# Kernel tuning notes

Measured on AMD Instinct MI355X. Metric: run time of the kernel, lower is better.

## Reference

```python
import jax, jax.numpy as jnp
import numpy as np
from jax import lax

BATCH, SEQ, D_FSQ = 8, 4096, 4
D_MODEL, D_STATE, D_CONV, L, OUT = 256, 16, 4, 2, 2
D_INNER = 2 * D_MODEL  # expand=2
EPS = 1e-5


def setup_inputs() -> dict:
    key = jax.random.key(0)
    ks = jax.random.split(key, 10)
    s = 0.02
    return {
        "z_seq": jax.random.normal(ks[0], (BATCH, SEQ, D_FSQ), jnp.float32),
        "ip_w": jax.random.normal(ks[1], (D_MODEL, D_FSQ), jnp.float32) * s,
        "ip_b": jnp.zeros((D_MODEL,), jnp.float32),
        "norm_g": jnp.ones((L, D_MODEL), jnp.float32),
        "norm_b": jnp.zeros((L, D_MODEL), jnp.float32),
        "inproj_w": jax.random.normal(ks[2], (L, 2 * D_INNER, D_MODEL), jnp.float32) * s,
        "conv_w": jax.random.normal(ks[3], (L, D_INNER, D_CONV), jnp.float32) * s,
        "conv_b": jnp.zeros((L, D_INNER), jnp.float32),
        "xproj_w": jax.random.normal(ks[4], (L, 2 * D_STATE + 1, D_INNER), jnp.float32) * s,
        "dt_w": jax.random.normal(ks[5], (L, D_INNER), jnp.float32) * s,
        "dt_b": jnp.zeros((L, D_INNER), jnp.float32),
        "outproj_w": jax.random.normal(ks[6], (L, D_MODEL, D_INNER), jnp.float32) * s,
        "onorm_g": jnp.ones((D_MODEL,), jnp.float32),
        "onorm_b": jnp.zeros((D_MODEL,), jnp.float32),
        "op_w": jax.random.normal(ks[7], (OUT, D_MODEL), jnp.float32) * s,
        "op_b": jnp.zeros((OUT,), jnp.float32),
    }


def _layernorm(x, g, b):
    mu = jnp.mean(x, axis=-1, keepdims=True)
    var = jnp.mean(jnp.square(x - mu), axis=-1, keepdims=True)
    return (x - mu) * lax.rsqrt(var + EPS) * g + b


def _selective_scan(x, dt, Bm, Cm):
    # x, dt: [B,T,d_inner]; Bm, Cm: [B,T,d_state]
    A = -jnp.arange(1, D_STATE + 1, dtype=x.dtype)  # [d_state]

    def step(h, inp):
        x_t, dt_t, B_t, C_t = inp  # [B,di],[B,di],[B,ds],[B,ds]
        A_bar = jnp.exp(dt_t[:, :, None] * A)            # [B,di,ds]
        h = A_bar * h + (dt_t * x_t)[:, :, None] * B_t[:, None, :]
        y_t = jnp.einsum("bds,bs->bd", h, C_t)
        return h, y_t

    xs = (jnp.swapaxes(x, 0, 1), jnp.swapaxes(dt, 0, 1),
          jnp.swapaxes(Bm, 0, 1), jnp.swapaxes(Cm, 0, 1))
    h0 = jnp.zeros((x.shape[0], D_INNER, D_STATE), x.dtype)
    _, ys = lax.scan(step, h0, xs)
    return jnp.swapaxes(ys, 0, 1)  # [B,T,d_inner]


def _block(x, g, b, Wi, cw, cb, Wx, dw, db, Wo):
    res = x
    x = _layernorm(x, g, b)
    xz = x @ Wi.T                               # [B,T,2*d_inner]
    xp, z = xz[..., :D_INNER], xz[..., D_INNER:]
    # causal depthwise conv1d (padding=d_conv-1 then truncate == left pad)
    xc = lax.conv_general_dilated(
        jnp.swapaxes(xp, 1, 2), cw[:, None, :], window_strides=(1,),
        padding=[(D_CONV - 1, 0)], dimension_numbers=("NCH", "OIH", "NCH"),
        feature_group_count=D_INNER) + cb[None, :, None]
    xc = jax.nn.silu(jnp.swapaxes(xc, 1, 2))    # [B,T,d_inner]
    ssm = xc @ Wx.T                             # [B,T,2*ds+1]
    Bm = ssm[..., :D_STATE]
    Cm = ssm[..., D_STATE:2 * D_STATE]
    dt_raw = ssm[..., 2 * D_STATE:]             # [B,T,1]
    dt = jax.nn.softplus(dt_raw * dw + db)      # Linear(1, d_inner)
    y = _selective_scan(xc, dt, Bm, Cm)
    y = y * jax.nn.silu(z)
    y = y @ Wo.T
    return y + res


def reference(z_seq, ip_w, ip_b, norm_g, norm_b, inproj_w, conv_w, conv_b,
              xproj_w, dt_w, dt_b, outproj_w, onorm_g, onorm_b, op_w, op_b):
    x = z_seq @ ip_w.T + ip_b
    for l in range(L):
        x = _block(x, norm_g[l], norm_b[l], inproj_w[l], conv_w[l], conv_b[l],
                   xproj_w[l], dt_w[l], dt_b[l], outproj_w[l])
    x = _layernorm(x, onorm_g, onorm_b)
    return x @ op_w.T + op_b
```

## Files before the change

### kernel.cpp

```cpp
#include <hip/hip_runtime.h>
#include <cstddef>
#include <cstdint>

#define DEV __device__ __forceinline__

namespace {
constexpr int BATCH = 8;
constexpr int SEQL  = 4096;
constexpr int DM    = 256;
constexpr int DS    = 16;
constexpr int DI    = 512;
constexpr int NTOK  = BATCH * SEQL;
constexpr int TC    = 64;
constexpr int NCH   = SEQL / TC;
constexpr float EPSF = 1e-5f;

constexpr size_t OFF_X   = 0;
constexpr size_t OFF_XPB = OFF_X   + (size_t)NTOK * DM * 4;
constexpr size_t OFF_ZBB = OFF_XPB + (size_t)NTOK * DI * 2;
constexpr size_t OFF_XCB = OFF_ZBB + (size_t)NTOK * DI * 2;
constexpr size_t OFF_XLN = OFF_XCB + (size_t)NTOK * DI * 2;
constexpr size_t OFF_B   = OFF_XLN + (size_t)NTOK * DM * 2;
constexpr size_t OFF_C   = OFF_B   + (size_t)NTOK * DS * 4;
constexpr size_t OFF_DTR = OFF_C   + (size_t)NTOK * DS * 4;
constexpr size_t OFF_HE  = OFF_DTR + (size_t)NTOK * 4;
constexpr size_t OFF_DTC = OFF_HE  + (size_t)BATCH * DI * NCH * DS * 4;
constexpr size_t OFF_WBI = OFF_DTC + (size_t)BATCH * DI * NCH * 4;
constexpr size_t OFF_WBO = OFF_WBI + (size_t)2 * 2 * DI * DM * 2;
constexpr size_t OFF_WBX = OFF_WBO + (size_t)2 * DM * DI * 2;
constexpr size_t OFF_CWT = OFF_WBX + (size_t)2 * 48 * DI * 2;
constexpr size_t WBI_EL  = 2 * 2 * DI * DM;
constexpr size_t WBO_EL  = 2 * DM * DI;
}

typedef __attribute__((ext_vector_type(8))) short short8;
typedef __attribute__((ext_vector_type(4))) float f32x4;

DEV float sigmoidf_(float v) { return 1.0f / (1.0f + __expf(-v)); }
DEV float siluf_(float v)    { return v * sigmoidf_(v); }
DEV float softplusf_(float v) {
    return fmaxf(v, 0.0f) + __logf(1.0f + __expf(-fabsf(v)));
}
DEV float b2f(unsigned short u) {
    union { unsigned int i; float f; } c; c.i = ((unsigned int)u) << 16; return c.f;
}
DEV float4 b4f(ushort4 u) {
    return make_float4(b2f(u.x), b2f(u.y), b2f(u.z), b2f(u.w));
}
DEV unsigned short f2b(float f) {
    union { float f; unsigned int i; } c; c.f = f;
    unsigned int lsb = (c.i >> 16) & 1u;
    c.i += 0x7fffu + lsb;
    return (unsigned short)(c.i >> 16);
}
DEV void pows16(float p, float* pb) {
    float p2 = p * p, p4 = p2 * p2, p8 = p4 * p4;
    pb[0] = p;        pb[1] = p2;       pb[2] = p2 * p;      pb[3] = p4;
    pb[4] = p4 * p;   pb[5] = p4 * p2;  pb[6] = p4 * p2 * p; pb[7] = p8;
    pb[8] = p8 * p;   pb[9] = p8 * p2;  pb[10] = p8 * p2 * p; pb[11] = p8 * p4;
    pb[12] = p8 * p4 * p; pb[13] = p8 * p4 * p2; pb[14] = p8 * p4 * p2 * p; pb[15] = p8 * p8;
}
DEV void gload_lds16(const unsigned short* g, unsigned short* l) {
    __builtin_amdgcn_global_load_lds(
        (__attribute__((address_space(1))) void*)(g),
        (__attribute__((address_space(3))) void*)(l), 16, 0, 0);
}

__global__ void k_cvt(const float* __restrict__ src, unsigned short* __restrict__ dst, int n) {
    int g = (blockIdx.x * 256 + threadIdx.x) * 4;
    if (g >= n) return;
    float4 v = *(const float4*)(src + g);
    ushort4 o;
    o.x = f2b(v.x); o.y = f2b(v.y); o.z = f2b(v.z); o.w = f2b(v.w);
    *(ushort4*)(dst + g) = o;
}

__global__ void k_cvtx(const float* __restrict__ src, unsigned short* __restrict__ dst) {
    int idx = blockIdx.x * 256 + threadIdx.x;
    int l = idx / (48 * 512), r = (idx >> 9) % 48, cc = idx & 511;
    dst[idx] = (r < 33) ? f2b(src[(size_t)(l * 33 + r) * 512 + cc]) : (unsigned short)0;
}

__global__ void k_cvtc(const float* __restrict__ src, float* __restrict__ dst) {
    int idx = blockIdx.x * 256 + threadIdx.x;
    int l = idx >> 11, k = (idx >> 9) & 3, d = idx & 511;
    dst[idx] = src[(size_t)(l * DI + d) * 4 + k];
}

__global__ void k_inproj(const float* __restrict__ z, const float* __restrict__ w,
                         const float* __restrict__ bias, float* __restrict__ x) {
    int g = blockIdx.x * 256 + threadIdx.x;
    int i = g >> 8, m = g & 255;
    float4 zv = *(const float4*)(z + (size_t)i * 4);
    float4 wv = *(const float4*)(w + (size_t)m * 4);
    float r = bias[m];
    r = fmaf(zv.x, wv.x, r);
    r = fmaf(zv.y, wv.y, r);
    r = fmaf(zv.z, wv.z, r);
    r = fmaf(zv.w, wv.w, r);
    x[g] = r;
}

__global__ void k_lnrow(const float* __restrict__ x, const float* __restrict__ gam,
                        const float* __restrict__ bet, unsigned short* __restrict__ xln) {
    int lane = threadIdx.x & 63, wid = threadIdx.x >> 6;
    int i = blockIdx.x * 4 + wid;
    float4 v = *(const float4*)(x + (size_t)i * DM + lane * 4);
    float s = v.x + v.y + v.z + v.w;
    float q = v.x * v.x + v.y * v.y + v.z * v.z + v.w * v.w;
    #pragma unroll
    for (int m = 32; m; m >>= 1) { s += __shfl_xor(s, m, 64); q += __shfl_xor(q, m, 64); }
    float mu = s * (1.0f / DM);
    float rs = rsqrtf(q * (1.0f / DM) - mu * mu + EPSF);
    float4 g4 = *(const float4*)(gam + lane * 4);
    float4 b4 = *(const float4*)(bet + lane * 4);
    ushort4 o;
    o.x = f2b((v.x - mu) * rs * g4.x + b4.x);
    o.y = f2b((v.y - mu) * rs * g4.y + b4.y);
    o.z = f2b((v.z - mu) * rs * g4.z + b4.z);
    o.w = f2b((v.w - mu) * rs * g4.w + b4.w);
    *(ushort4*)(xln + (size_t)i * DM + lane * 4) = o;
}

__global__ __launch_bounds__(256) void k_gemm1(
    const unsigned short* __restrict__ A, const unsigned short* __restrict__ W,
    unsigned short* __restrict__ xpb, unsigned short* __restrict__ zbb) {
    __shared__ unsigned short As[128 * 32];
    __shared__ unsigned short Bs[128 * 32];
    int tid = threadIdx.x, lane = tid & 63, wid = tid >> 6;
    int tileN = blockIdx.x & 7, tileM = blockIdx.x >> 3;
    int i0 = tileM * 128, n0 = tileN * 128;
    f32x4 acc[4][4];
    #pragma unroll
    for (int mi = 0; mi < 4; mi++)
        #pragma unroll
        for (int ni = 0; ni < 4; ni++) acc[mi][ni] = (f32x4){0.f, 0.f, 0.f, 0.f};

    int srow = (wid << 5) + (lane >> 2);
    int sblk = lane & 3;
    const unsigned short* ga = A + (size_t)(i0 + srow) * 256 + sblk * 8;
    const unsigned short* gb = W + (size_t)(n0 + srow) * 256 + sblk * 8;
    unsigned short* la = As + (wid << 5) * 32;
    unsigned short* lb = Bs + (wid << 5) * 32;
    int ar = lane & 15, ab = lane >> 4;
    const short8* pa = (const short8*)(As + ((wid >> 1) * 64 + ar) * 32 + ab * 8);
    const short8* pb = (const short8*)(Bs + ((wid & 1) * 64 + ar) * 32 + ab * 8);

    for (int k0 = 0; k0 < 256; k0 += 32) {
        gload_lds16(ga + k0,            la);
        gload_lds16(ga + k0 + 16 * 256, la + 16 * 32);
        gload_lds16(gb + k0,            lb);
        gload_lds16(gb + k0 + 16 * 256, lb + 16 * 32);
        __syncthreads();
        short8 a[4], b[4];
        #pragma unroll
        for (int mi = 0; mi < 4; mi++) a[mi] = pa[mi * 64];
        #pragma unroll
        for (int ni = 0; ni < 4; ni++) b[ni] = pb[ni * 64];
        #pragma unroll
        for (int mi = 0; mi < 4; mi++)
            #pragma unroll
            for (int ni = 0; ni < 4; ni++)
                acc[mi][ni] = __builtin_amdgcn_mfma_f32_16x16x32_bf16(a[mi], b[ni], acc[mi][ni], 0, 0, 0);
        __syncthreads();
    }
    int wr = wid >> 1, wc = wid & 1;
    int rbase = i0 + wr * 64 + (lane >> 4) * 4;
    int cbase = n0 + wc * 64 + (lane & 15);
    unsigned short* dst = (n0 < 512) ? xpb : zbb;
    int coff = (n0 < 512) ? cbase : cbase - 512;
    #pragma unroll
    for (int mi = 0; mi < 4; mi++)
        #pragma unroll
        for (int ni = 0; ni < 4; ni++)
            #pragma unroll
            for (int j = 0; j < 4; j++)
                dst[(size_t)(rbase + mi * 16 + j) * 512 + coff + ni * 16] = f2b(acc[mi][ni][j]);
}

__global__ void k_conv(const unsigned short* __restrict__ xpb, const float* __restrict__ cwT,
                       const float* __restrict__ cb, unsigned short* __restrict__ xcb) {
    int g = blockIdx.x * 256 + threadIdx.x;
    int tg = g >> 7, dq = g & 127;
    int d = dq * 4;
    int i0 = tg * 8;
    float4 w0 = *(const float4*)(cwT + 0 * DI + d);
    float4 w1 = *(const float4*)(cwT + 1 * DI + d);
    float4 w2 = *(const float4*)(cwT + 2 * DI + d);
    float4 w3 = *(const float4*)(cwT + 3 * DI + d);
    float4 bi = *(const float4*)(cb + d);
    float4 x0, x1, x2;
    if ((i0 & (SEQL - 1)) != 0) {
        x0 = b4f(*(const ushort4*)(xpb + (size_t)(i0 - 3) * DI + d));
        x1 = b4f(*(const ushort4*)(xpb + (size_t)(i0 - 2) * DI + d));
        x2 = b4f(*(const ushort4*)(xpb + (size_t)(i0 - 1) * DI + d));
    } else {
        x0 = x1 = x2 = make_float4(0.f, 0.f, 0.f, 0.f);
    }
    #pragma unroll
    for (int tt = 0; tt < 8; tt++) {
        float4 xc = b4f(*(const ushort4*)(xpb + (size_t)(i0 + tt) * DI + d));
        float4 a = bi;
        a.x = fmaf(w0.x, x0.x, a.x); a.y = fmaf(w0.y, x0.y, a.y);
        a.z = fmaf(w0.z, x0.z, a.z); a.w = fmaf(w0.w, x0.w, a.w);
        a.x = fmaf(w1.x, x1.x, a.x); a.y = fmaf(w1.y, x1.y, a.y);
        a.z = fmaf(w1.z, x1.z, a.z); a.w = fmaf(w1.w, x1.w, a.w);
        a.x = fmaf(w2.x, x2.x, a.x); a.y = fmaf(w2.y, x2.y, a.y);
        a.z = fmaf(w2.z, x2.z, a.z); a.w = fmaf(w2.w, x2.w, a.w);
        a.x = fmaf(w3.x, xc.x, a.x); a.y = fmaf(w3.y, xc.y, a.y);
        a.z = fmaf(w3.z, xc.z, a.z); a.w = fmaf(w3.w, xc.w, a.w);
        ushort4 o;
        o.x = f2b(siluf_(a.x)); o.y = f2b(siluf_(a.y));
        o.z = f2b(siluf_(a.z)); o.w = f2b(siluf_(a.w));
        *(ushort4*)(xcb + (size_t)(i0 + tt) * DI + d) = o;
        x0 = x1; x1 = x2; x2 = xc;
    }
}

__global__ __launch_bounds__(256) void k_xprojm(
    const unsigned short* __restrict__ A, const unsigned short* __restrict__ W,
    float* __restrict__ Bm, float* __restrict__ Cm, float* __restrict__ dtr) {
    __shared__ unsigned short As[128 * 32];
    __shared__ unsigned short Bs[48 * 32];
    int tid = threadIdx.x, lane = tid & 63, wid = tid >> 6;
    int i0 = blockIdx.x * 128;
    f32x4 acc[2][3];
    #pragma unroll
    for (int mi = 0; mi < 2; mi++)
        #pragma unroll
        for (int ni = 0; ni < 3; ni++) acc[mi][ni] = (f32x4){0.f, 0.f, 0.f, 0.f};

    int srow = lane >> 2, sblk = lane & 3;
    const unsigned short* ga = A + (size_t)(i0 + (wid << 5) + srow) * 512 + sblk * 8;
    unsigned short* la = As + (wid << 5) * 32;
    const unsigned short* gb = W + (size_t)((wid << 4) + srow) * 512 + sblk * 8;
    unsigned short* lb = Bs + (wid << 4) * 32;
    int ar = lane & 15, ab = lane >> 4;

    for (int k0 = 0; k0 < 512; k0 += 32) {
        gload_lds16(ga + k0,            la);
        gload_lds16(ga + k0 + 16 * 512, la + 16 * 32);
        if (wid < 3) gload_lds16(gb + k0, lb);
        __syncthreads();
        short8 a[2], b[3];
        #pragma unroll
        for (int mi = 0; mi < 2; mi++)
            a[mi] = *(const short8*)(As + ((wid << 5) + mi * 16 + ar) * 32 + ab * 8);
        #pragma unroll
        for (int ni = 0; ni < 3; ni++)
            b[ni] = *(const short8*)(Bs + (ni * 16 + ar) * 32 + ab * 8);
        #pragma unroll
        for (int mi = 0; mi < 2; mi++)
            #pragma unroll
            for (int ni = 0; ni < 3; ni++)
                acc[mi][ni] = __builtin_amdgcn_mfma_f32_16x16x32_bf16(a[mi], b[ni], acc[mi][ni], 0, 0, 0);
        __syncthreads();
    }
    #pragma unroll
    for (int mi = 0; mi < 2; mi++)
        #pragma unroll
        for (int ni = 0; ni < 3; ni++)
            #pragma unroll
            for (int j = 0; j < 4; j++) {
                int row = i0 + (wid << 5) + mi * 16 + (lane >> 4) * 4 + j;
                int ng = ni * 16 + (lane & 15);
                float v = acc[mi][ni][j];
                if (ng < 16)       Bm[(size_t)row * DS + ng] = v;
                else if (ng < 32)  Cm[(size_t)row * DS + ng - 16] = v;
                else if (ng == 32) dtr[row] = v;
            }
}

__global__ __launch_bounds__(256) void k_scan1(
    const unsigned short* __restrict__ xcb, const float* __restrict__ Bm,
    const float* __restrict__ dtr, const float* __restrict__ dw,
    const float* __restrict__ db, float* __restrict__ hend, float* __restrict__ dtc) {
    __shared__ float Bsh[64][16];
    __shared__ float dtl[64];
    int tid = threadIdx.x;
    int blk = blockIdx.x;
    int half = blk & 1, c = (blk >> 1) & (NCH - 1), b = blk >> 7;
    int d = half * 256 + tid;
    int i0 = (b << 12) + c * TC;
    if (tid < 64) dtl[tid] = dtr[i0 + tid];
    {
        int idx = tid * 4, tt = idx >> 4, ss = idx & 15;
        *(float4*)(&Bsh[tt][ss]) = *(const float4*)(Bm + (size_t)(i0 + tt) * DS + ss);
    }
    __syncthreads();
    float dwd = dw[d], dbd = db[d];
    float h[16];
    #pragma unroll
    for (int s = 0; s < 16; s++) h[s] = 0.0f;
    float dtsum = 0.0f;
    for (int t = 0; t < TC; t++) {
        float dt = softplusf_(fmaf(dtl[t], dwd, dbd));
        dtsum += dt;
        float p = __expf(-dt);
        float pb[16];
        pows16(p, pb);
        float x = b2f(xcb[(size_t)(i0 + t) * DI + d]);
        float dtx = dt * x;
        float Bv[16];
        *(float4*)(Bv + 0)  = *(const float4*)(&Bsh[t][0]);
        *(float4*)(Bv + 4)  = *(const float4*)(&Bsh[t][4]);
        *(float4*)(Bv + 8)  = *(const float4*)(&Bsh[t][8]);
        *(float4*)(Bv + 12) = *(const float4*)(&Bsh[t][12]);
        #pragma unroll
        for (int s = 0; s < 16; s++) h[s] = fmaf(pb[s], h[s], dtx * Bv[s]);
    }
    size_t hb = ((size_t)(b * DI + d) * NCH + c) * DS;
    #pragma unroll
    for (int s = 0; s < 16; s += 4)
        *(float4*)(hend + hb + s) = make_float4(h[s], h[s + 1], h[s + 2], h[s + 3]);
    dtc[(size_t)(b * DI + d) * NCH + c] = dtsum;
}

__global__ void k_scan2(float* __restrict__ hend, const float* __restrict__ dtc) {
    int g = blockIdx.x * 256 + threadIdx.x;
    int s = g & 15, dd = (g >> 4) & 511, b = g >> 13;
    size_t base = (size_t)(b * DI + dd) * NCH;
    float hin = 0.0f;
    float kneg = -(float)(s + 1);
    #pragma unroll 4
    for (int c = 0; c < NCH; c++) {
        size_t a = (base + c) * DS + s;
        float tmp = hend[a];
        float pb = __expf(kneg * dtc[base + c]);
        hend[a] = hin;
        hin = fmaf(pb, hin, tmp);
    }
}

__global__ __launch_bounds__(256) void k_scan3(
    const unsigned short* __restrict__ xcb, const float* __restrict__ Bm,
    const float* __restrict__ Cm, const float* __restrict__ dtr,
    const float* __restrict__ dw, const float* __restrict__ db,
    const float* __restrict__ hend, const unsigned short* __restrict__ zbb,
    unsigned short* __restrict__ ygb) {
    __shared__ float Bsh[64][16];
    __shared__ float Csh[64][16];
    __shared__ float dtl[64];
    int tid = threadIdx.x;
    int blk = blockIdx.x;
    int half = blk & 1, c = (blk >> 1) & (NCH - 1), b = blk >> 7;
    int d = half * 256 + tid;
    int i0 = (b << 12) + c * TC;
    if (tid < 64) dtl[tid] = dtr[i0 + tid];
    {
        int idx = tid * 4, tt = idx >> 4, ss = idx & 15;
        *(float4*)(&Bsh[tt][ss]) = *(const float4*)(Bm + (size_t)(i0 + tt) * DS + ss);
        *(float4*)(&Csh[tt][ss]) = *(const float4*)(Cm + (size_t)(i0 + tt) * DS + ss);
    }
    __syncthreads();
    float dwd = dw[d], dbd = db[d];
    float h[16];
    size_t hb = ((size_t)(b * DI + d) * NCH + c) * DS;
    #pragma unroll
    for (int s = 0; s < 16; s += 4) *(float4*)(h + s) = *(const float4*)(hend + hb + s);
    for (int t = 0; t < TC; t++) {
        float dt = softplusf_(fmaf(dtl[t], dwd, dbd));
        float p = __expf(-dt);
        float pb[16];
        pows16(p, pb);
        size_t gi = (size_t)(i0 + t) * DI + d;
        float x = b2f(xcb[gi]);
        float dtx = dt * x;
        float Bv[16], Cv[16];
        *(float4*)(Bv + 0)  = *(const float4*)(&Bsh[t][0]);
        *(float4*)(Bv + 4)  = *(const float4*)(&Bsh[t][4]);
        *(float4*)(Bv + 8)  = *(const float4*)(&Bsh[t][8]);
        *(float4*)(Bv + 12) = *(const float4*)(&Bsh[t][12]);
        *(float4*)(Cv + 0)  = *(const float4*)(&Csh[t][0]);
        *(float4*)(Cv + 4)  = *(const float4*)(&Csh[t][4]);
        *(float4*)(Cv + 8)  = *(const float4*)(&Csh[t][8]);
        *(float4*)(Cv + 12) = *(const float4*)(&Csh[t][12]);
        float y = 0.0f;
        #pragma unroll
        for (int s = 0; s < 16; s++) {
            h[s] = fmaf(pb[s], h[s], dtx * Bv[s]);
            y = fmaf(h[s], Cv[s], y);
        }
        float z = b2f(zbb[gi]);
        ygb[gi] = f2b(y * siluf_(z));
    }
}

__global__ __launch_bounds__(256) void k_outproj(
    const unsigned short* __restrict__ A, const unsigned short* __restrict__ W,
    float* __restrict__ x) {
    __shared__ unsigned short As[128 * 32];
    __shared__ unsigned short Bs[128 * 32];
    int tid = threadIdx.x, lane = tid & 63, wid = tid >> 6;
    int tileN = blockIdx.x & 1, tileM = blockIdx.x >> 1;
    int i0 = tileM * 128, n0 = tileN * 128;
    f32x4 acc[4][4];
    #pragma unroll
    for (int mi = 0; mi < 4; mi++)
        #pragma unroll
        for (int ni = 0; ni < 4; ni++) acc[mi][ni] = (f32x4){0.f, 0.f, 0.f, 0.f};

    int srow = (wid << 5) + (lane >> 2);
    int sblk = lane & 3;
    const unsigned short* ga = A + (size_t)(i0 + srow) * 512 + sblk * 8;
    const unsigned short* gb = W + (size_t)(n0 + srow) * 512 + sblk * 8;
    unsigned short* la = As + (wid << 5) * 32;
    unsigned short* lb = Bs + (wid << 5) * 32;
    int ar = lane & 15, ab = lane >> 4;
    const short8* pa = (const short8*)(As + ((wid >> 1) * 64 + ar) * 32 + ab * 8);
    const short8* pb = (const short8*)(Bs + ((wid & 1) * 64 + ar) * 32 + ab * 8);

    for (int k0 = 0; k0 < 512; k0 += 32) {
        gload_lds16(ga + k0,            la);
        gload_lds16(ga + k0 + 16 * 512, la + 16 * 32);
        gload_lds16(gb + k0,            lb);
        gload_lds16(gb + k0 + 16 * 512, lb + 16 * 32);
        __syncthreads();
        short8 a[4], b[4];
        #pragma unroll
        for (int mi = 0; mi < 4; mi++) a[mi] = pa[mi * 64];
        #pragma unroll
        for (int ni = 0; ni < 4; ni++) b[ni] = pb[ni * 64];
        #pragma unroll
        for (int mi = 0; mi < 4; mi++)
            #pragma unroll
            for (int ni = 0; ni < 4; ni++)
                acc[mi][ni] = __builtin_amdgcn_mfma_f32_16x16x32_bf16(a[mi], b[ni], acc[mi][ni], 0, 0, 0);
        __syncthreads();
    }
    int wr = wid >> 1, wc = wid & 1;
    int rbase = i0 + wr * 64 + (lane >> 4) * 4;
    int cbase = n0 + wc * 64 + (lane & 15);
    #pragma unroll
    for (int mi = 0; mi < 4; mi++)
        #pragma unroll
        for (int ni = 0; ni < 4; ni++)
            #pragma unroll
            for (int j = 0; j < 4; j++) {
                size_t idx = (size_t)(rbase + mi * 16 + j) * DM + cbase + ni * 16;
                x[idx] += acc[mi][ni][j];
            }
}

__global__ void k_final(const float* __restrict__ x, const float* __restrict__ gam,
                        const float* __restrict__ bet, const float* __restrict__ w,
                        const float* __restrict__ bias, float* __restrict__ out) {
    int lane = threadIdx.x & 63, wid = threadIdx.x >> 6;
    int i = blockIdx.x * 4 + wid;
    float4 v = *(const float4*)(x + (size_t)i * DM + lane * 4);
    float s = v.x + v.y + v.z + v.w;
    float q = v.x * v.x + v.y * v.y + v.z * v.z + v.w * v.w;
    #pragma unroll
    for (int m = 32; m; m >>= 1) { s += __shfl_xor(s, m, 64); q += __shfl_xor(q, m, 64); }
    float mu = s * (1.0f / DM);
    float rs = rsqrtf(q * (1.0f / DM) - mu * mu + EPSF);
    float4 gg = *(const float4*)(gam + lane * 4);
    float4 bb = *(const float4*)(bet + lane * 4);
    float xn[4] = {(v.x - mu) * rs * gg.x + bb.x, (v.y - mu) * rs * gg.y + bb.y,
                   (v.z - mu) * rs * gg.z + bb.z, (v.w - mu) * rs * gg.w + bb.w};
    float4 w0 = *(const float4*)(w + lane * 4);
    float4 w1 = *(const float4*)(w + DM + lane * 4);
    float p0 = xn[0] * w0.x + xn[1] * w0.y + xn[2] * w0.z + xn[3] * w0.w;
    float p1 = xn[0] * w1.x + xn[1] * w1.y + xn[2] * w1.z + xn[3] * w1.w;
    #pragma unroll
    for (int m = 32; m; m >>= 1) { p0 += __shfl_xor(p0, m, 64); p1 += __shfl_xor(p1, m, 64); }
    if (lane == 0) {
        out[(size_t)i * 2]     = p0 + bias[0];
        out[(size_t)i * 2 + 1] = p1 + bias[1];
    }
}

extern "C" void kernel_launch(void* const* d_in, const int* in_sizes, int n_in,
                              void* d_out, int out_size, void* d_ws, size_t ws_size,
                              hipStream_t stream) {
    const float* z_seq     = (const float*)d_in[0];
    const float* ip_w      = (const float*)d_in[1];
    const float* ip_b      = (const float*)d_in[2];
    const float* norm_g    = (const float*)d_in[3];
    const float* norm_b    = (const float*)d_in[4];
    const float* inproj_w  = (const float*)d_in[5];
    const float* conv_w    = (const float*)d_in[6];
    const float* conv_b    = (const float*)d_in[7];
    const float* xproj_w   = (const float*)d_in[8];
    const float* dt_w      = (const float*)d_in[9];
    const float* dt_b      = (const float*)d_in[10];
    const float* outproj_w = (const float*)d_in[11];
    const float* onorm_g   = (const float*)d_in[12];
    const float* onorm_b   = (const float*)d_in[13];
    const float* op_w      = (const float*)d_in[14];
    const float* op_b      = (const float*)d_in[15];

    char* ws = (char*)d_ws;
    float* x    = (float*)(ws + OFF_X);
    unsigned short* xpb = (unsigned short*)(ws + OFF_XPB);
    unsigned short* zbb = (unsigned short*)(ws + OFF_ZBB);
    unsigned short* xcb = (unsigned short*)(ws + OFF_XCB);
    unsigned short* xln = (unsigned short*)(ws + OFF_XLN);
    float* Bmb  = (float*)(ws + OFF_B);
    float* Cmb  = (float*)(ws + OFF_C);
    float* dtrb = (float*)(ws + OFF_DTR);
    float* hend = (float*)(ws + OFF_HE);
    float* dtc  = (float*)(ws + OFF_DTC);
    unsigned short* WbI = (unsigned short*)(ws + OFF_WBI);
    unsigned short* WbO = (unsigned short*)(ws + OFF_WBO);
    unsigned short* WbX = (unsigned short*)(ws + OFF_WBX);
    float* cwT  = (float*)(ws + OFF_CWT);

    k_cvt<<<(int)(WBI_EL / 4 / 256), 256, 0, stream>>>(inproj_w,  WbI, (int)WBI_EL);
    k_cvt<<<(int)(WBO_EL / 4 / 256), 256, 0, stream>>>(outproj_w, WbO, (int)WBO_EL);
    k_cvtx<<<2 * 48 * 512 / 256, 256, 0, stream>>>(xproj_w, WbX);
    k_cvtc<<<2 * 4 * 512 / 256, 256, 0, stream>>>(conv_w, cwT);

    k_inproj<<<NTOK * DM / 256, 256, 0, stream>>>(z_seq, ip_w, ip_b, x);

    for (int l = 0; l < 2; l++) {
        k_lnrow<<<NTOK / 4, 256, 0, stream>>>(x, norm_g + l * DM, norm_b + l * DM, xln);
        k_gemm1<<<(NTOK / 128) * 8, 256, 0, stream>>>(
            xln, WbI + (size_t)l * 2 * DI * DM, xpb, zbb);
        k_conv<<<(NTOK / 8) * 128 / 256, 256, 0, stream>>>(
            xpb, cwT + (size_t)l * 4 * DI, conv_b + (size_t)l * DI, xcb);
        k_xprojm<<<NTOK / 128, 256, 0, stream>>>(
            xcb, WbX + (size_t)l * 48 * DI, Bmb, Cmb, dtrb);
        k_scan1<<<BATCH * NCH * 2, 256, 0, stream>>>(
            xcb, Bmb, dtrb, dt_w + l * DI, dt_b + l * DI, hend, dtc);
        k_scan2<<<BATCH * DI * DS / 256, 256, 0, stream>>>(hend, dtc);
        k_scan3<<<BATCH * NCH * 2, 256, 0, stream>>>(
            xcb, Bmb, Cmb, dtrb, dt_w + l * DI, dt_b + l * DI, hend, zbb, xpb);
        k_outproj<<<(NTOK / 128) * 2, 256, 0, stream>>>(
            xpb, WbO + (size_t)l * DM * DI, x);
    }
    k_final<<<NTOK / 4, 256, 0, stream>>>(x, onorm_g, onorm_b, op_w, op_b, (float*)d_out);
}
```

Measured before the change: 509.0 us.

## Halve scan chunk length, simplify softplus/exp, fuse weight prep kernels

Chunk length for the chunked selective scan drops from 64 to 32 tokens, doubling the number of scan blocks to raise parallelism in scan1/scan3, at the cost of a longer sequential pass in scan2. Softplus plus exp(-dt) is replaced by computing p = 1/(1+e^a) and dt = -log p, which saves transcendental instructions per step. Launch bounds with an occupancy hint are added to the scan kernels. The four weight-conversion launches are merged into one k_prep kernel to cut launch overhead.

```diff
diff --git a/kernel.cpp b/kernel.cpp
--- a/kernel.cpp
+++ b/kernel.cpp
@@ -11,7 +11,7 @@
 constexpr int DS    = 16;
 constexpr int DI    = 512;
 constexpr int NTOK  = BATCH * SEQL;
-constexpr int TC    = 64;
+constexpr int TC    = 32;
 constexpr int NCH   = SEQL / TC;
 constexpr float EPSF = 1e-5f;
 
@@ -31,6 +31,10 @@
 constexpr size_t OFF_CWT = OFF_WBX + (size_t)2 * 48 * DI * 2;
 constexpr size_t WBI_EL  = 2 * 2 * DI * DM;
 constexpr size_t WBO_EL  = 2 * DM * DI;
+constexpr int PREP_T1 = (int)(WBI_EL / 4);
+constexpr int PREP_T2 = PREP_T1 + (int)(WBO_EL / 4);
+constexpr int PREP_T3 = PREP_T2 + 2 * 48 * 512;
+constexpr int PREP_T4 = PREP_T3 + 2 * 4 * 512;
 }
 
 typedef __attribute__((ext_vector_type(8))) short short8;
@@ -38,9 +42,6 @@
 
 DEV float sigmoidf_(float v) { return 1.0f / (1.0f + __expf(-v)); }
 DEV float siluf_(float v)    { return v * sigmoidf_(v); }
-DEV float softplusf_(float v) {
-    return fmaxf(v, 0.0f) + __logf(1.0f + __expf(-fabsf(v)));
-}
 DEV float b2f(unsigned short u) {
     union { unsigned int i; float f; } c; c.i = ((unsigned int)u) << 16; return c.f;
 }
@@ -52,6 +53,10 @@
     unsigned int lsb = (c.i >> 16) & 1u;
     c.i += 0x7fffu + lsb;
     return (unsigned short)(c.i >> 16);
+}
+DEV void dt_p_(float a, float& dt, float& p) {
+    p = __builtin_amdgcn_rcpf(1.0f + __expf(a));
+    dt = -__logf(p);
 }
 DEV void pows16(float p, float* pb) {
     float p2 = p * p, p4 = p2 * p2, p8 = p4 * p4;
@@ -66,25 +71,36 @@
         (__attribute__((address_space(3))) void*)(l), 16, 0, 0);
 }
 
-__global__ void k_cvt(const float* __restrict__ src, unsigned short* __restrict__ dst, int n) {
-    int g = (blockIdx.x * 256 + threadIdx.x) * 4;
-    if (g >= n) return;
-    float4 v = *(const float4*)(src + g);
-    ushort4 o;
-    o.x = f2b(v.x); o.y = f2b(v.y); o.z = f2b(v.z); o.w = f2b(v.w);
-    *(ushort4*)(dst + g) = o;
-}
-
-__global__ void k_cvtx(const float* __restrict__ src, unsigned short* __restrict__ dst) {
+__global__ void k_prep(const float* __restrict__ inproj_w, const float* __restrict__ outproj_w,
+                       const float* __restrict__ xproj_w, const float* __restrict__ conv_w,
+                       unsigned short* __restrict__ WbI, unsigned short* __restrict__ WbO,
+                       unsigned short* __restrict__ WbX, float* __restrict__ cwT) {
     int idx = blockIdx.x * 256 + threadIdx.x;
-    int l = idx / (48 * 512), r = (idx >> 9) % 48, cc = idx & 511;
-    dst[idx] = (r < 33) ? f2b(src[(size_t)(l * 33 + r) * 512 + cc]) : (unsigned short)0;
-}
-
-__global__ void k_cvtc(const float* __restrict__ src, float* __restrict__ dst) {
-    int idx = blockIdx.x * 256 + threadIdx.x;
-    int l = idx >> 11, k = (idx >> 9) & 3, d = idx & 511;
-    dst[idx] = src[(size_t)(l * DI + d) * 4 + k];
+    if (idx < PREP_T1) {
+        int g = idx * 4;
+        float4 v = *(const float4*)(inproj_w + g);
+        ushort4 o; o.x = f2b(v.x); o.y = f2b(v.y); o.z = f2b(v.z); o.w = f2b(v.w);
+        *(ushort4*)(WbI + g) = o;
+        return;
+    }
+    if (idx < PREP_T2) {
+        int g = (idx - PREP_T1) * 4;
+        float4 v = *(const float4*)(outproj_w + g);
+        ushort4 o; o.x = f2b(v.x); o.y = f2b(v.y); o.z = f2b(v.z); o.w = f2b(v.w);
+        *(ushort4*)(WbO + g) = o;
+        return;
+    }
+    if (idx < PREP_T3) {
+        int q = idx - PREP_T2;
+        int l = q / (48 * 512), r = (q >> 9) % 48, cc = q & 511;
+        WbX[q] = (r < 33) ? f2b(xproj_w[(size_t)(l * 33 + r) * 512 + cc]) : (unsigned short)0;
+        return;
+    }
+    if (idx < PREP_T4) {
+        int q = idx - PREP_T3;
+        int l = q >> 11, k = (q >> 9) & 3, d = q & 511;
+        cwT[q] = conv_w[(size_t)(l * DI + d) * 4 + k];
+    }
 }
 
 __global__ void k_inproj(const float* __restrict__ z, const float* __restrict__ w,
@@ -271,20 +287,20 @@
             }
 }
 
-__global__ __launch_bounds__(256) void k_scan1(
+__global__ __launch_bounds__(256, 8) void k_scan1(
     const unsigned short* __restrict__ xcb, const float* __restrict__ Bm,
     const float* __restrict__ dtr, const float* __restrict__ dw,
     const float* __restrict__ db, float* __restrict__ hend, float* __restrict__ dtc) {
-    __shared__ float Bsh[64][16];
-    __shared__ float dtl[64];
+    __shared__ float Bsh[TC][16];
+    __shared__ float dtl[TC];
     int tid = threadIdx.x;
     int blk = blockIdx.x;
-    int half = blk & 1, c = (blk >> 1) & (NCH - 1), b = blk >> 7;
+    int half = blk & 1, c = (blk >> 1) & (NCH - 1), b = blk >> 8;
     int d = half * 256 + tid;
     int i0 = (b << 12) + c * TC;
-    if (tid < 64) dtl[tid] = dtr[i0 + tid];
-    {
-        int idx = tid * 4, tt = idx >> 4, ss = idx & 15;
+    if (tid < TC) dtl[tid] = dtr[i0 + tid];
+    if (tid < TC * 4) {
+        int tt = tid >> 2, ss = (tid & 3) * 4;
         *(float4*)(&Bsh[tt][ss]) = *(const float4*)(Bm + (size_t)(i0 + tt) * DS + ss);
     }
     __syncthreads();
@@ -292,13 +308,11 @@
     float h[16];
     #pragma unroll
     for (int s = 0; s < 16; s++) h[s] = 0.0f;
-    float dtsum = 0.0f;
+    float dts = 0.0f;
     for (int t = 0; t < TC; t++) {
-        float dt = softplusf_(fmaf(dtl[t], dwd, dbd));
-        dtsum += dt;
-        float p = __expf(-dt);
-        float pb[16];
-        pows16(p, pb);
+        float dt, p;
+        dt_p_(fmaf(dtl[t], dwd, dbd), dt, p);
+        dts += dt;
         float x = b2f(xcb[(size_t)(i0 + t) * DI + d]);
         float dtx = dt * x;
         float Bv[16];
@@ -306,6 +320,8 @@
         *(float4*)(Bv + 4)  = *(const float4*)(&Bsh[t][4]);
         *(float4*)(Bv + 8)  = *(const float4*)(&Bsh[t][8]);
         *(float4*)(Bv + 12) = *(const float4*)(&Bsh[t][12]);
+        float pb[16];
+        pows16(p, pb);
         #pragma unroll
         for (int s = 0; s < 16; s++) h[s] = fmaf(pb[s], h[s], dtx * Bv[s]);
     }
@@ -313,7 +329,7 @@
     #pragma unroll
     for (int s = 0; s < 16; s += 4)
         *(float4*)(hend + hb + s) = make_float4(h[s], h[s + 1], h[s + 2], h[s + 3]);
-    dtc[(size_t)(b * DI + d) * NCH + c] = dtsum;
+    dtc[(size_t)(b * DI + d) * NCH + c] = dts;
 }
 
 __global__ void k_scan2(float* __restrict__ hend, const float* __restrict__ dtc) {
@@ -332,24 +348,27 @@
     }
 }
 
-__global__ __launch_bounds__(256) void k_scan3(
+__global__ __launch_bounds__(256, 8) void k_scan3(
     const unsigned short* __restrict__ xcb, const float* __restrict__ Bm,
     const float* __restrict__ Cm, const float* __restrict__ dtr,
     const float* __restrict__ dw, const float* __restrict__ db,
     const float* __restrict__ hend, const unsigned short* __restrict__ zbb,
     unsigned short* __restrict__ ygb) {
-    __shared__ float Bsh[64][16];
-    __shared__ float Csh[64][16];
-    __shared__ float dtl[64];
+    __shared__ float Bsh[TC][16];
+    __shared__ float Csh[TC][16];
+    __shared__ float dtl[TC];
     int tid = threadIdx.x;
     int blk = blockIdx.x;
-    int half = blk & 1, c = (blk >> 1) & (NCH - 1), b = blk >> 7;
+    int half = blk & 1, c = (blk >> 1) & (NCH - 1), b = blk >> 8;
     int d = half * 256 + tid;
     int i0 = (b << 12) + c * TC;
-    if (tid < 64) dtl[tid] = dtr[i0 + tid];
-    {
-        int idx = tid * 4, tt = idx >> 4, ss = idx & 15;
+    if (tid < TC) dtl[tid] = dtr[i0 + tid];
+    if (tid < TC * 4) {
+        int tt = tid >> 2, ss = (tid & 3) * 4;
         *(float4*)(&Bsh[tt][ss]) = *(const float4*)(Bm + (size_t)(i0 + tt) * DS + ss);
+    } else if (tid < TC * 8) {
+        int q = tid - TC * 4;
+        int tt = q >> 2, ss = (q & 3) * 4;
         *(float4*)(&Csh[tt][ss]) = *(const float4*)(Cm + (size_t)(i0 + tt) * DS + ss);
     }
     __syncthreads();
@@ -359,10 +378,8 @@
     #pragma unroll
     for (int s = 0; s < 16; s += 4) *(float4*)(h + s) = *(const float4*)(hend + hb + s);
     for (int t = 0; t < TC; t++) {
-        float dt = softplusf_(fmaf(dtl[t], dwd, dbd));
-        float p = __expf(-dt);
-        float pb[16];
-        pows16(p, pb);
+        float dt, p;
+        dt_p_(fmaf(dtl[t], dwd, dbd), dt, p);
         size_t gi = (size_t)(i0 + t) * DI + d;
         float x = b2f(xcb[gi]);
         float dtx = dt * x;
@@ -375,6 +392,8 @@
         *(float4*)(Cv + 4)  = *(const float4*)(&Csh[t][4]);
         *(float4*)(Cv + 8)  = *(const float4*)(&Csh[t][8]);
         *(float4*)(Cv + 12) = *(const float4*)(&Csh[t][12]);
+        float pb[16];
+        pows16(p, pb);
         float y = 0.0f;
         #pragma unroll
         for (int s = 0; s < 16; s++) {
@@ -506,11 +525,8 @@
     unsigned short* WbX = (unsigned short*)(ws + OFF_WBX);
     float* cwT  = (float*)(ws + OFF_CWT);
 
-    k_cvt<<<(int)(WBI_EL / 4 / 256), 256, 0, stream>>>(inproj_w,  WbI, (int)WBI_EL);
-    k_cvt<<<(int)(WBO_EL / 4 / 256), 256, 0, stream>>>(outproj_w, WbO, (int)WBO_EL);
-    k_cvtx<<<2 * 48 * 512 / 256, 256, 0, stream>>>(xproj_w, WbX);
-    k_cvtc<<<2 * 4 * 512 / 256, 256, 0, stream>>>(conv_w, cwT);
-
+    k_prep<<<PREP_T4 / 256, 256, 0, stream>>>(inproj_w, outproj_w, xproj_w, conv_w,
+                                              WbI, WbO, WbX, cwT);
     k_inproj<<<NTOK * DM / 256, 256, 0, stream>>>(z_seq, ip_w, ip_b, x);
 
     for (int l = 0; l < 2; l++) {
```

After: 522.5 us. +2.6%, slower.
